# Performance work log

Measured on AMD Instinct MI355X. Metric: run time of the kernel, lower is better.

## Reference

```python
import jax, jax.numpy as jnp
import numpy as np

D_MODEL = 1024
NUM_HEADS = 16
DILATION_RATES = [2, 2, 2]
SEGMENT_SIZES = [64, 128, 256]
BATCH = 2
SEQ_LEN = 8192
N_LAYERS = len(SEGMENT_SIZES)


def setup_inputs() -> dict:
    key = jax.random.key(0)
    ks = jax.random.split(key, 5)
    d = D_MODEL
    scale = 1.0 / np.sqrt(d)
    x = jax.random.normal(ks[0], (BATCH, SEQ_LEN, d), dtype=jnp.float32)
    # Per-layer fused QKV + output projection params (stacked over layers)
    Wqkv = jax.random.normal(ks[1], (N_LAYERS, d, 3 * d), dtype=jnp.float32) * scale
    bqkv = jnp.zeros((N_LAYERS, 3 * d), dtype=jnp.float32)
    Wo = jax.random.normal(ks[2], (N_LAYERS, d, d), dtype=jnp.float32) * scale
    bo = jnp.zeros((N_LAYERS, d), dtype=jnp.float32)
    return {"x": x, "Wqkv": Wqkv, "bqkv": bqkv, "Wo": Wo, "bo": bo}


def _dilated_attention(x, Wqkv, bqkv, Wo, bo, seg, dr):
    # x: [B, S, D]. Segment, then dilate-stride within each segment.
    B, S, D = x.shape
    H = NUM_HEADS
    hd = D // H
    x4 = x.reshape(B, S // seg, seg, D)[:, :, ::dr, :]  # [B, N, s, D], s = seg//dr
    s = seg // dr
    N = S // seg
    qkv = jnp.einsum('bnsd,de->bnse', x4, Wqkv) + bqkv  # [B, N, s, 3D]
    q, k, v = jnp.split(qkv, 3, axis=-1)
    q = q.reshape(B, N, s, H, hd)
    k = k.reshape(B, N, s, H, hd)
    v = v.reshape(B, N, s, H, hd)
    # attention within each dilated segment
    scores = jnp.einsum('bnqhd,bnkhd->bnhqk', q, k) * (1.0 / np.sqrt(hd))
    attn = jax.nn.softmax(scores, axis=-1)
    o = jnp.einsum('bnhqk,bnkhd->bnqhd', attn, v).reshape(B, N, s, D)
    o = jnp.einsum('bnsd,de->bnse', o, Wo) + bo
    return o.reshape(B, N * s, D)  # [B, S/dr, D]


def reference(x, Wqkv, bqkv, Wo, bo):
    outs = []
    for i in range(N_LAYERS):
        outs.append(_dilated_attention(x, Wqkv[i], bqkv[i], Wo[i], bo[i],
                                       SEGMENT_SIZES[i], DILATION_RATES[i]))
    return jnp.stack(outs, axis=0).sum(axis=0)
```

## Files before the change

kernel.cpp:

```cpp
#include <hip/hip_runtime.h>
#include <hip/hip_bf16.h>
#include <stdint.h>

typedef unsigned short u16;
typedef short bf16x8 __attribute__((ext_vector_type(8)));
typedef u16   u16x8  __attribute__((ext_vector_type(8)));
typedef u16   u16x4  __attribute__((ext_vector_type(4)));
typedef float f32x4  __attribute__((ext_vector_type(4)));

__device__ inline u16 f2bf(float f) {
    uint32_t u = __builtin_bit_cast(uint32_t, f);
    uint32_t r = (u + 0x7FFFu + ((u >> 16) & 1u)) >> 16;
    return (u16)r;
}

__device__ inline void gload16(const void* g, void* l) {
    __builtin_amdgcn_global_load_lds((const __attribute__((address_space(1))) void*)g,
                                     (__attribute__((address_space(3))) void*)l, 16, 0, 0);
}

__device__ inline void pin_barrier() {
    __builtin_amdgcn_sched_barrier(0);
    __builtin_amdgcn_s_barrier();
    __builtin_amdgcn_sched_barrier(0);
}

#define MFMA16(a, b, c) __builtin_amdgcn_mfma_f32_16x16x32_bf16((a), (b), (c), 0, 0, 0)

__global__ __launch_bounds__(256) void k_prep_xe(const float* __restrict__ x,
                                                 u16* __restrict__ xe) {
    int row = blockIdx.x;
    int b = row >> 12, tt = row & 4095;
    const float* src = x + ((size_t)b * 8192 + 2 * (size_t)tt) * 1024;
    float4 v = ((const float4*)src)[threadIdx.x];
    u16x4 o = { f2bf(v.x), f2bf(v.y), f2bf(v.z), f2bf(v.w) };
    *(u16x4*)(xe + (size_t)row * 1024 + threadIdx.x * 4) = o;
}

__global__ __launch_bounds__(256) void k_transpose_cast(
    const float* __restrict__ src, u16* __restrict__ dst,
    int srcCols, size_t srcLayerStride, int dstStride, int dstRowPer, int dstColPer) {
    int k0 = blockIdx.x * 64, e0 = blockIdx.y * 64, layer = blockIdx.z;
    const float* s = src + (size_t)layer * srcLayerStride;
    __shared__ u16 T[64][66];
    int t = threadIdx.x;
#pragma unroll
    for (int p = 0; p < 16; ++p) {
        int l = p * 256 + t;
        int kl = l >> 6, el = l & 63;
        T[kl][el] = f2bf(s[(size_t)(k0 + kl) * srcCols + e0 + el]);
    }
    __syncthreads();
    int rowBase = layer * dstRowPer + e0;
    int colBase = layer * dstColPer + k0;
#pragma unroll
    for (int p = 0; p < 16; ++p) {
        int l = p * 256 + t;
        int eo = l >> 6, ko = l & 63;
        dst[(size_t)(rowBase + eo) * dstStride + colBase + ko] = T[ko][eo];
    }
}

template <int BN, bool BF16OUT>
__global__ __launch_bounds__(512, 2) void k_gemm5(
    const u16* __restrict__ A, const u16* __restrict__ B, void* __restrict__ C,
    const float* __restrict__ bias0, const float* __restrict__ bias1,
    const float* __restrict__ bias2, int K, int lda, int ldb, int ldc,
    int gxmask, int gxshift) {
    constexpr int WN = BN / 64;
    constexpr int WM = 8 / WN;
    constexpr int MFRAG = 256 / (WM * 16);
    constexpr int NBB = BN / 128;
    constexpr int NL = 2 + NBB;
    constexpr int BUFSZ = 16384 + BN * 64;

    __shared__ __align__(16) char smem[131072];
    const int tid = threadIdx.x, lane = tid & 63, wave = tid >> 6;
    const int wr = wave / WN, wc = wave % WN;

    const int nwg = gridDim.x, bid = blockIdx.x;
    const int cpx = nwg >> 3;
    const int swz = (bid & 7) * cpx + (bid >> 3);
    const int bx = swz & gxmask, by = swz >> gxshift;
    const int row0 = bx << 8, col0 = by * BN;

    const size_t lda2 = (size_t)lda * 2, ldb2 = (size_t)ldb * 2;
    const int cSw = ((tid & 3) ^ ((tid >> 3) & 3)) * 16;
    const char* pA0 = (const char*)A + (size_t)(row0 + (tid >> 2)) * lda2 + cSw;
    const char* pB0 = (const char*)B + (size_t)(col0 + (tid >> 2)) * ldb2 + cSw;

#define STA(i, sb, kof) gload16(pA0 + (size_t)(i) * 128 * lda2 + (kof), \
                                (sb) + (i) * 8192 + wave * 1024)
#define STB(i, sb, kof) gload16(pB0 + (size_t)(i) * 128 * ldb2 + (kof), \
                                (sb) + 16384 + (i) * 8192 + wave * 1024)
#define STAGE_ALL(sb, kof) do { \
        STA(0, sb, kof); STA(1, sb, kof); \
        STB(0, sb, kof); if constexpr (NBB == 2) STB(1, sb, kof); } while (0)

    auto WAIT_VM = [] {
        if constexpr (NL == 4) asm volatile("s_waitcnt vmcnt(8)" ::: "memory");
        else                   asm volatile("s_waitcnt vmcnt(6)" ::: "memory");
    };

    const int lane_off = (lane & 15) * 64 +
                         (((lane >> 4) ^ (((lane & 15) >> 1) & 3)) << 4);

    f32x4 acc[MFRAG][4] = {};
    const int nt = K >> 5;

#define TILE_BODY(q, q3, t) do { \
        char* rq = smem + (q) * BUFSZ; \
        char* sq = smem + (q3) * BUFSZ; \
        const char* aRd = rq + wr * (MFRAG * 1024) + lane_off; \
        const char* bRd = rq + 16384 + wc * 4096 + lane_off; \
        bf16x8 af[4], bg[4]; \
        _Pragma("unroll") for (int n = 0; n < 4; ++n) \
            bg[n] = *(const bf16x8*)(bRd + n * 1024); \
        _Pragma("unroll") for (int m = 0; m < 4; ++m) \
            af[m] = *(const bf16x8*)(aRd + m * 1024); \
        {  \
            const int ts = ((t) + 3 < nt) ? (t) + 3 : nt - 1; \
            const size_t kof = (size_t)ts * 64; \
            STAGE_ALL(sq, kof); \
        } \
        bf16x8 ag[4]; \
        if constexpr (MFRAG == 8) { \
            _Pragma("unroll") for (int m = 0; m < 4; ++m) \
                ag[m] = *(const bf16x8*)(aRd + (4 + m) * 1024); \
        } \
        __builtin_amdgcn_sched_barrier(0); \
        __builtin_amdgcn_s_setprio(1); \
        _Pragma("unroll") for (int m = 0; m < 4; ++m) \
            _Pragma("unroll") for (int n = 0; n < 4; ++n) \
                acc[m][n] = MFMA16(af[m], bg[n], acc[m][n]); \
        __builtin_amdgcn_s_setprio(0); \
        if constexpr (MFRAG == 8) { \
            __builtin_amdgcn_sched_barrier(0); \
            __builtin_amdgcn_s_setprio(1); \
            _Pragma("unroll") for (int m = 0; m < 4; ++m) \
                _Pragma("unroll") for (int n = 0; n < 4; ++n) \
                    acc[4 + m][n] = MFMA16(ag[m], bg[n], acc[4 + m][n]); \
            __builtin_amdgcn_s_setprio(0); \
        } \
        __builtin_amdgcn_sched_barrier(0); \
        WAIT_VM(); \
        pin_barrier(); \
    } while (0)

    STAGE_ALL(smem + 0 * BUFSZ, 0);
    STAGE_ALL(smem + 1 * BUFSZ, 64);
    STAGE_ALL(smem + 2 * BUFSZ, 128);
    __builtin_amdgcn_sched_barrier(0);
    WAIT_VM();
    pin_barrier();

    for (int t = 0; t < nt; t += 4) {
        TILE_BODY(0, 3, t + 0);
        TILE_BODY(1, 0, t + 1);
        TILE_BODY(2, 1, t + 2);
        TILE_BODY(3, 2, t + 3);
    }
#undef TILE_BODY
#undef STAGE_ALL
#undef STA
#undef STB

    {
        char* cst = smem;
        const int g4 = (lane >> 4) << 2, cl = lane & 15;
        __builtin_amdgcn_sched_barrier(0);
        asm volatile("s_waitcnt vmcnt(0)" ::: "memory");
        pin_barrier();
#pragma unroll
        for (int n = 0; n < 4; ++n) {
            int col = wc * 64 + n * 16 + cl;
            float bs = bias0[col0 + col];
            if (bias1) bs += bias1[col0 + col];
            if (bias2) bs += bias2[col0 + col];
#pragma unroll
            for (int m = 0; m < MFRAG; ++m) {
#pragma unroll
                for (int r = 0; r < 4; ++r) {
                    int row = wr * (MFRAG * 16) + m * 16 + g4 + r;
                    float v = acc[m][n][r] + bs;
                    if (BF16OUT) {
                        int scol = col ^ (((row >> 2) & 3) << 3);
                        *(u16*)(cst + row * 512 + scol * 2) = f2bf(v);
                    } else {
                        int scol = col ^ (((row >> 2) & 3) << 2);
                        *(float*)(cst + row * 512 + scol * 4) = v;
                    }
                }
            }
        }
        pin_barrier();
        const int esz = BF16OUT ? 2 : 4;
#pragma unroll
        for (int it = 0; it < 16; ++it) {
            int id = it * 512 + tid;
            int row = id >> 5, c16 = id & 31;
            int sc16 = c16 ^ ((row >> 2) & 3);
            u16x8 v = *(const u16x8*)(cst + row * 512 + sc16 * 16);
            char* dst = (char*)C + ((size_t)(row0 + row) * ldc + col0) * esz + c16 * 16;
            *(u16x8*)dst = v;
        }
    }
}

template <int S>
__global__ __launch_bounds__(256) void k_attn(const u16* __restrict__ qkv,
                                              u16* __restrict__ ab, int layer) {
    constexpr int NCT = S / 16;
    constexpr int RPW = (S == 32) ? 1 : S / 64;
    constexpr int ACTIVE = (S == 32) ? 2 : 4;
    constexpr int KST = S / 32;
    constexpr int VSTRIDE = 2 * S;
    constexpr int VMASK = VSTRIDE / 16 - 1;

    __shared__ __align__(16) char KS[S * 128];
    __shared__ __align__(16) char VTS[64 * VSTRIDE];
    __shared__ __align__(16) char PS[S * VSTRIDE];

    const int per_b = (4096 / S) * 16;
    const int b = blockIdx.x / per_b;
    const int r0 = blockIdx.x % per_b;
    const int n = r0 >> 4, h = r0 & 15;
    const int token0 = b * 4096 + n * S;
    const int colQ = layer * 3072 + h * 64;
    const int tid = threadIdx.x, lane = tid & 63, wave = tid >> 6;

    constexpr int CHUNKS = S / 32;
#pragma unroll
    for (int c = 0; c < CHUNKS; ++c) {
        int lc = c * 256 + tid;
        int row = lc >> 3, off = (lc & 7) * 16;
        const char* base = (const char*)qkv + ((size_t)(token0 + row) * 9216 + colQ) * 2 + off;
        u16x8 kv = *(const u16x8*)(base + 1024 * 2);
        *(u16x8*)(KS + row * 128 + (off ^ ((row & 7) << 4))) = kv;
        u16x8 vv = *(const u16x8*)(base + 2048 * 2);
        int cb = off >> 1;
#pragma unroll
        for (int e = 0; e < 8; ++e) {
            int col = cb + e;
            *(u16*)(VTS + col * VSTRIDE + ((row * 2) ^ ((col & VMASK) << 4))) = vv[e];
        }
    }
    __syncthreads();

    f32x4 sacc[RPW][NCT] = {};
    if (wave < ACTIVE) {
#pragma unroll
        for (int rl = 0; rl < RPW; ++rl) {
            int rt = wave * RPW + rl;
#pragma unroll
            for (int ks2 = 0; ks2 < 2; ++ks2) {
                int qrow = token0 + rt * 16 + (lane & 15);
                int kbyte = ks2 * 64 + ((lane >> 4) << 4);
                bf16x8 aq = *(const bf16x8*)((const char*)qkv +
                              ((size_t)qrow * 9216 + colQ) * 2 + kbyte);
#pragma unroll
                for (int ct = 0; ct < NCT; ++ct) {
                    int krow = ct * 16 + (lane & 15);
                    bf16x8 bk = *(const bf16x8*)(KS + krow * 128 + (kbyte ^ ((krow & 7) << 4)));
                    sacc[rl][ct] = MFMA16(aq, bk, sacc[rl][ct]);
                }
            }
        }
#pragma unroll
        for (int rl = 0; rl < RPW; ++rl) {
            int rt = wave * RPW + rl;
#pragma unroll
            for (int r = 0; r < 4; ++r) {
                float vals[NCT];
                float m = -1e30f;
#pragma unroll
                for (int ct = 0; ct < NCT; ++ct) {
                    vals[ct] = sacc[rl][ct][r] * 0.125f;
                    m = fmaxf(m, vals[ct]);
                }
#pragma unroll
                for (int d = 1; d < 16; d <<= 1) m = fmaxf(m, __shfl_xor(m, d, 64));
                float sum = 0.f;
#pragma unroll
                for (int ct = 0; ct < NCT; ++ct) {
                    float p = exp2f((vals[ct] - m) * 1.44269504f);
                    vals[ct] = p;
                    sum += p;
                }
#pragma unroll
                for (int d = 1; d < 16; d <<= 1) sum += __shfl_xor(sum, d, 64);
                float inv = 1.0f / sum;
                int row = rt * 16 + ((lane >> 4) << 2) + r;
#pragma unroll
                for (int ct = 0; ct < NCT; ++ct) {
                    int col = ct * 16 + (lane & 15);
                    *(u16*)(PS + row * VSTRIDE + ((col * 2) ^ ((row & VMASK) << 4))) =
                        f2bf(vals[ct] * inv);
                }
            }
        }
    }
    __syncthreads();

    if (wave < ACTIVE) {
        const int colA = layer * 1024 + h * 64;
#pragma unroll
        for (int rl = 0; rl < RPW; ++rl) {
            int rt = wave * RPW + rl;
            f32x4 oacc[4] = {};
#pragma unroll
            for (int ks2 = 0; ks2 < KST; ++ks2) {
                int kbyte = ks2 * 64 + ((lane >> 4) << 4);
                int prow = rt * 16 + (lane & 15);
                bf16x8 ap = *(const bf16x8*)(PS + prow * VSTRIDE + (kbyte ^ ((prow & VMASK) << 4)));
#pragma unroll
                for (int ct = 0; ct < 4; ++ct) {
                    int vcol = ct * 16 + (lane & 15);
                    bf16x8 bv = *(const bf16x8*)(VTS + vcol * VSTRIDE + (kbyte ^ ((vcol & VMASK) << 4)));
                    oacc[ct] = MFMA16(ap, bv, oacc[ct]);
                }
            }
#pragma unroll
            for (int ct = 0; ct < 4; ++ct) {
#pragma unroll
                for (int r = 0; r < 4; ++r) {
                    int row = token0 + rt * 16 + ((lane >> 4) << 2) + r;
                    int col = colA + ct * 16 + (lane & 15);
                    ab[(size_t)row * 3072 + col] = f2bf(oacc[ct][r]);
                }
            }
        }
    }
}

extern "C" void kernel_launch(void* const* d_in, const int* in_sizes, int n_in,
                              void* d_out, int out_size, void* d_ws, size_t ws_size,
                              hipStream_t stream) {
    const float* x    = (const float*)d_in[0];
    const float* Wqkv = (const float*)d_in[1];
    const float* bqkv = (const float*)d_in[2];
    const float* Wo   = (const float*)d_in[3];
    const float* bo   = (const float*)d_in[4];

    char* ws = (char*)d_ws;
    u16* XE    = (u16*)(ws);
    u16* WQKVT = (u16*)(ws + 16777216);
    u16* WOT   = (u16*)(ws + 35651584);
    u16* QKVB  = (u16*)(ws + 41943040);
    u16* ABUF  = (u16*)(ws + 192937984);

    k_prep_xe<<<8192, 256, 0, stream>>>(x, XE);
    k_transpose_cast<<<dim3(16, 48, 3), 256, 0, stream>>>(
        Wqkv, WQKVT, 3072, (size_t)1024 * 3072, 1024, 3072, 0);
    k_transpose_cast<<<dim3(16, 16, 3), 256, 0, stream>>>(
        Wo, WOT, 1024, (size_t)1024 * 1024, 3072, 0, 1024);

    k_gemm5<256, true><<<dim3(1152), 512, 0, stream>>>(
        XE, WQKVT, QKVB, bqkv, nullptr, nullptr, 1024, 1024, 1024, 9216, 31, 5);

    k_attn<32><<<4096, 256, 0, stream>>>(QKVB, ABUF, 0);
    k_attn<64><<<2048, 256, 0, stream>>>(QKVB, ABUF, 1);
    k_attn<128><<<1024, 256, 0, stream>>>(QKVB, ABUF, 2);

    k_gemm5<128, false><<<dim3(256), 512, 0, stream>>>(
        ABUF, WOT, d_out, bo, bo + 1024, bo + 2048, 3072, 3072, 3072, 1024, 31, 5);
}
```

Before: 326.9 us.

## Replace QKV GEMM with 256x256 tile kernel using 4-phase split loads

Adds a new GEMM kernel for the QKV projection that keeps a 256x256 output tile with a K-step of 64, double-buffered in LDS. Each K step is split into four quadrant phases, and each phase issues one slice of the next tile's global-to-LDS loads and then runs its MFMAs. The aim is to overlap memory traffic with compute more evenly and to cut LDS fragment reloads. The epilogue stages results through swizzled LDS so the bf16 stores to global memory are coalesced. The cost is many more barriers per K step and higher register pressure from 32 accumulator fragments.

Result: no change. 333.3 us (+1.9%).

```diff
diff --git a/kernel.cpp b/kernel.cpp
--- a/kernel.cpp
+++ b/kernel.cpp
@@ -58,6 +58,134 @@
         int l = p * 256 + t;
         int eo = l >> 6, ko = l & 63;
         dst[(size_t)(rowBase + eo) * dstStride + colBase + ko] = T[ko][eo];
+    }
+}
+
+__global__ __launch_bounds__(512, 2) void k_gemm8(
+    const u16* __restrict__ A, const u16* __restrict__ B, u16* __restrict__ C,
+    const float* __restrict__ bias, int K, int lda, int ldb, int ldc,
+    int gxmask, int gxshift) {
+    __shared__ __align__(16) char smem[131072];
+    const int tid = threadIdx.x, lane = tid & 63, wave = tid >> 6;
+    const int wr = wave >> 1, wc = wave & 1;
+
+    const int nwg = gridDim.x, bid = blockIdx.x;
+    const int cpx = nwg >> 3;
+    const int swz = (bid & 7) * cpx + (bid >> 3);
+    const int bx = swz & gxmask, by = swz >> gxshift;
+    const int row0 = bx << 8, col0 = by << 8;
+
+    const size_t lda2 = (size_t)lda * 2, ldb2 = (size_t)ldb * 2;
+
+    const char* pA[2]; const char* pB[2];
+#pragma unroll
+    for (int i = 0; i < 2; ++i) {
+        int c = tid + i * 512;
+        int rl = c >> 3;
+        int chunk = (c & 4) + ((c & 3) ^ ((c >> 4) & 3));
+        pA[i] = (const char*)A + (size_t)(row0 + rl) * lda2 + chunk * 16;
+        pB[i] = (const char*)B + (size_t)(col0 + rl) * ldb2 + chunk * 16;
+    }
+    const int dstOff = tid * 16;
+
+    const int la = lane & 15, lg = lane >> 4;
+    int loff[2];
+#pragma unroll
+    for (int kh = 0; kh < 2; ++kh)
+        loff[kh] = la * 128 + ((kh * 4 + (lg ^ ((la >> 1) & 3))) << 4);
+
+    f32x4 acc[4][2][4] = {};
+    bf16x8 afr[2][2], bfr[4][2];
+    const int nt = K >> 6;
+
+#define ST_UA0(sb, kof) do { gload16(pA[0] + (kof), (sb) + dstOff); \
+                             gload16(pA[1] + (kof), (sb) + 8192 + dstOff); } while (0)
+#define ST_UB0(sb, kof) do { gload16(pB[0] + (kof), (sb) + 32768 + dstOff); \
+                             gload16(pB[1] + (kof), (sb) + 40960 + dstOff); } while (0)
+#define ST_UA1(sb, kof) do { gload16(pA[0] + (size_t)128 * lda2 + (kof), (sb) + 16384 + dstOff); \
+                             gload16(pA[1] + (size_t)128 * lda2 + (kof), (sb) + 24576 + dstOff); } while (0)
+#define ST_UB1(sb, kof) do { gload16(pB[0] + (size_t)128 * ldb2 + (kof), (sb) + 49152 + dstOff); \
+                             gload16(pB[1] + (size_t)128 * ldb2 + (kof), (sb) + 57344 + dstOff); } while (0)
+
+#define PHASE(p, RM, RN, rb, STG) do { \
+        if ((p) != 2) { \
+            _Pragma("unroll") for (int m = 0; m < 2; ++m) \
+            _Pragma("unroll") for (int kh = 0; kh < 2; ++kh) \
+                afr[m][kh] = *(const bf16x8*)((rb) + ((RM) + wr * 32 + m * 16) * 128 + loff[kh]); \
+        } \
+        if ((p) == 0 || (p) == 2) { \
+            _Pragma("unroll") for (int n = 0; n < 4; ++n) \
+            _Pragma("unroll") for (int kh = 0; kh < 2; ++kh) \
+                bfr[n][kh] = *(const bf16x8*)((rb) + 32768 + ((RN) + wc * 64 + n * 16) * 128 + loff[kh]); \
+        } \
+        STG; \
+        __builtin_amdgcn_sched_barrier(0); \
+        asm volatile("s_waitcnt vmcnt(4)" ::: "memory"); \
+        pin_barrier(); \
+        asm volatile("s_waitcnt lgkmcnt(0)" ::: "memory"); \
+        __builtin_amdgcn_sched_barrier(0); \
+        __builtin_amdgcn_s_setprio(1); \
+        _Pragma("unroll") for (int m = 0; m < 2; ++m) \
+        _Pragma("unroll") for (int n = 0; n < 4; ++n) \
+        _Pragma("unroll") for (int kh = 0; kh < 2; ++kh) \
+            acc[p][m][n] = MFMA16(afr[m][kh], bfr[n][kh], acc[p][m][n]); \
+        __builtin_amdgcn_s_setprio(0); \
+        pin_barrier(); \
+    } while (0)
+
+    ST_UA0(smem, 0); ST_UB0(smem, 0); ST_UA1(smem, 0); ST_UB1(smem, 0);
+    __builtin_amdgcn_sched_barrier(0);
+    asm volatile("s_waitcnt vmcnt(4)" ::: "memory");
+    pin_barrier();
+
+    for (int t = 0; t < nt; ++t) {
+        char* rb = smem + (t & 1) * 65536;
+        char* sb = smem + ((t & 1) ^ 1) * 65536;
+        const size_t kof = (size_t)((t + 1 < nt) ? t + 1 : nt - 1) * 128;
+        PHASE(0,   0,   0, rb, ST_UA0(sb, kof));
+        PHASE(1, 128,   0, rb, ST_UB0(sb, kof));
+        PHASE(2, 128, 128, rb, ST_UA1(sb, kof));
+        PHASE(3,   0, 128, rb, ST_UB1(sb, kof));
+    }
+#undef PHASE
+#undef ST_UA0
+#undef ST_UB0
+#undef ST_UA1
+#undef ST_UB1
+
+    {
+        char* cst = smem;
+        __builtin_amdgcn_sched_barrier(0);
+        asm volatile("s_waitcnt vmcnt(0)" ::: "memory");
+        pin_barrier();
+        const int g4 = lg << 2;
+        const int RMv[4] = {0, 128, 128, 0}, RNv[4] = {0, 0, 128, 128};
+#pragma unroll
+        for (int p = 0; p < 4; ++p) {
+#pragma unroll
+            for (int n = 0; n < 4; ++n) {
+                int col = RNv[p] + wc * 64 + n * 16 + la;
+                float bs = bias[col0 + col];
+#pragma unroll
+                for (int m = 0; m < 2; ++m) {
+#pragma unroll
+                    for (int r = 0; r < 4; ++r) {
+                        int row = RMv[p] + wr * 32 + m * 16 + g4 + r;
+                        int scol = col ^ (((row >> 2) & 3) << 3);
+                        *(u16*)(cst + row * 512 + scol * 2) = f2bf(acc[p][m][n][r] + bs);
+                    }
+                }
+            }
+        }
+        pin_barrier();
+#pragma unroll
+        for (int it = 0; it < 16; ++it) {
+            int id = it * 512 + tid;
+            int r2 = id >> 5, c16 = id & 31;
+            int sc16 = c16 ^ ((r2 >> 2) & 3);
+            u16x8 v = *(const u16x8*)(cst + r2 * 512 + sc16 * 16);
+            *(u16x8*)((char*)C + ((size_t)(row0 + r2) * ldc + col0) * 2 + c16 * 16) = v;
+        }
     }
 }
 
@@ -118,7 +246,7 @@
             bg[n] = *(const bf16x8*)(bRd + n * 1024); \
         _Pragma("unroll") for (int m = 0; m < 4; ++m) \
             af[m] = *(const bf16x8*)(aRd + m * 1024); \
-        {  \
+        { \
             const int ts = ((t) + 3 < nt) ? (t) + 3 : nt - 1; \
             const size_t kof = (size_t)ts * 64; \
             STAGE_ALL(sq, kof); \
@@ -355,8 +483,8 @@
     k_transpose_cast<<<dim3(16, 16, 3), 256, 0, stream>>>(
         Wo, WOT, 1024, (size_t)1024 * 1024, 3072, 0, 1024);
 
-    k_gemm5<256, true><<<dim3(1152), 512, 0, stream>>>(
-        XE, WQKVT, QKVB, bqkv, nullptr, nullptr, 1024, 1024, 1024, 9216, 31, 5);
+    k_gemm8<<<dim3(1152), 512, 0, stream>>>(
+        XE, WQKVT, QKVB, bqkv, 1024, 1024, 1024, 9216, 31, 5);
 
     k_attn<32><<<4096, 256, 0, stream>>>(QKVB, ABUF, 0);
     k_attn<64><<<2048, 256, 0, stream>>>(QKVB, ABUF, 1);
```
